# Performance work log

Measured on AMD Instinct MI355X. Metric: run time of the kernel, lower is better.

Reference implementation:

```python
import jax, jax.numpy as jnp
import numpy as np

TOP_K = 2
SCALING = 16.0 / 8.0  # alpha / rank


def setup_inputs() -> dict:
    key = jax.random.key(0)
    ks = jax.random.split(key, 9)
    B, V, D, P = 32, 21, 512, 64
    IN, OUT, E, R, H = D * P, 96, 8, 8, 256
    return {
        "x": jax.random.normal(ks[0], (B, V, D, P), jnp.float32),
        "W_base": jax.random.normal(ks[1], (OUT, IN), jnp.float32) * (IN ** -0.5),
        "b_base": jax.random.normal(ks[2], (OUT,), jnp.float32) * 0.01,
        "W1": jax.random.normal(ks[3], (H, D), jnp.float32) * (D ** -0.5),
        "b1": jax.random.normal(ks[4], (H,), jnp.float32) * 0.01,
        "W2": jax.random.normal(ks[5], (E, H), jnp.float32) * (H ** -0.5),
        "b2": jax.random.normal(ks[6], (E,), jnp.float32) * 0.01,
        "lora_A": jax.random.normal(ks[7], (E, R, IN), jnp.float32) * (IN ** -0.5),
        "lora_B": jax.random.normal(ks[8], (E, OUT, R), jnp.float32) * (R ** -0.5),
    }


def reference(x, W_base, b_base, W1, b1, W2, b2, lora_A, lora_B):
    B, V, D, P = x.shape
    E = lora_A.shape[0]
    # FlattenHead: flatten last two dims, then linear (dropout is identity in eval)
    flat = x.reshape(B, V, D * P)                      # [B, V, IN]
    base_out = flat @ W_base.T + b_base                # [B, V, OUT]
    # Router: pool over n_vars then patch dim -> [B, D]
    pooled = x.mean(axis=1).mean(axis=-1)
    h = jax.nn.relu(pooled @ W1.T + b1)
    logits = h @ W2.T + b2                             # [B, E]
    probs = jax.nn.softmax(logits, axis=-1)
    topw, topi = jax.lax.top_k(probs, TOP_K)           # [B, K]
    topw = topw / jnp.clip(topw.sum(-1, keepdims=True), 1e-6)
    # All LoRA experts (matches original dense compute), then weighted combine
    temp = jnp.einsum("bvi,eri->ebvr", flat, lora_A)   # [E, B, V, R]
    delta = jnp.einsum("ebvr,eor->ebvo", temp, lora_B) * SCALING  # [E, B, V, OUT]
    # Scatter top-k weights into dense [B, E] then combine (top-k sparse combine)
    w_full = jnp.zeros((B, E), x.dtype).at[jnp.arange(B)[:, None], topi].add(topw)
    moe_delta = jnp.einsum("be,ebvo->bvo", w_full, delta)
    return base_out + moe_delta, probs
```

## Files before the change

### kernel.cpp

```cpp
#include <hip/hip_runtime.h>

#define B_DIM 32
#define V_DIM 21
#define D_DIM 512
#define P_DIM 64
#define M_TOTAL 672
#define K_TOTAL 32768
#define OUT_DIM 96
#define E_DIM 8
#define R_DIM 8
#define H_DIM 256
#define N_TOTAL 160
#define SCALING 2.0f
#define POOL_SCALE (1.0f / (V_DIM * (float)P_DIM))

#define BM 64
#define BK 64
#define KSPLIT 64
#define K_PER_SPLIT (K_TOTAL / KSPLIT)
#define CHUNKS (K_PER_SPLIT / BK)
#define LDS_K (BK + 8)
#define SMN (M_TOTAL * N_TOTAL)
#define RC_ROWS 2

typedef __attribute__((ext_vector_type(4))) float floatx4;
typedef __attribute__((ext_vector_type(8))) short short8;
typedef __attribute__((ext_vector_type(4))) short shortx4;

__device__ __forceinline__ unsigned short f2bf(float f) {
  union { float f; unsigned int u; } v; v.f = f;
  unsigned int u = v.u + (0x7FFFu + ((v.u >> 16) & 1u));
  return (unsigned short)(u >> 16);
}

__global__ __launch_bounds__(256)
void convW_kernel(const float* __restrict__ W_base, const float* __restrict__ lora_A,
                  short* __restrict__ Wb, float* __restrict__ pooled) {
  int gid = blockIdx.x * 256 + threadIdx.x;
  if (blockIdx.x < 64) pooled[gid] = 0.0f;
  size_t base = (size_t)gid * 8;
  int row = (int)(base >> 15);
  int k = (int)(base & 32767);
  const float* src = (row < OUT_DIM) ? (W_base + ((size_t)row << 15) + k)
                                     : (lora_A + ((size_t)(row - OUT_DIM) << 15) + k);
  floatx4 v0 = ((const floatx4*)src)[0];
  floatx4 v1 = ((const floatx4*)src)[1];
  short8 sv;
  sv[0] = (short)f2bf(v0[0]); sv[1] = (short)f2bf(v0[1]);
  sv[2] = (short)f2bf(v0[2]); sv[3] = (short)f2bf(v0[3]);
  sv[4] = (short)f2bf(v1[0]); sv[5] = (short)f2bf(v1[1]);
  sv[6] = (short)f2bf(v1[2]); sv[7] = (short)f2bf(v1[3]);
  *(short8*)(Wb + base) = sv;
}

__global__ __launch_bounds__(256, 4)
void gemm_kernel(const float* __restrict__ x, const short* __restrict__ Wb,
                 float* __restrict__ P, float* __restrict__ pooled) {
  __shared__ short ldsA[BM * LDS_K];
  __shared__ short ldsB[N_TOTAL * LDS_K];
  __shared__ float lds_pool[5 * 8];
  const int tid = threadIdx.x;
  const int m0 = blockIdx.x * BM;
  const int ky = blockIdx.y;
  const int kbase = ky * K_PER_SPLIT;
  const int lane = tid & 63;
  const int wave = tid >> 6;
  const int quad = lane >> 4;
  const int l16 = lane & 15;
  const int b_first = m0 / V_DIM;
  const int d_first = kbase >> 6;

  if (tid < 40) lds_pool[tid] = 0.0f;

  floatx4 acc[10];
  #pragma unroll
  for (int nt = 0; nt < 10; ++nt) acc[nt] = (floatx4)(0.0f);

  floatx4 pa[4];
  short8 pb[5];

#define ISSUE(c)                                                                \
  {                                                                             \
    const int kc = kbase + (c) * BK;                                            \
    _Pragma("unroll")                                                           \
    for (int it = 0; it < 4; ++it) {                                            \
      int idx = it * 256 + tid;                                                 \
      int arow = idx >> 4;                                                      \
      int u = idx & 15;                                                         \
      int m = m0 + arow;                                                        \
      pa[it] = (m < M_TOTAL)                                                    \
          ? *(const floatx4*)(x + (size_t)m * K_TOTAL + kc + u * 4)             \
          : (floatx4)(0.0f);                                                    \
    }                                                                           \
    _Pragma("unroll")                                                           \
    for (int it = 0; it < 5; ++it) {                                            \
      int idx = it * 256 + tid;                                                 \
      int brow = idx >> 3;                                                      \
      int g = idx & 7;                                                          \
      pb[it] = *(const short8*)(Wb + (size_t)brow * K_TOTAL + kc + g * 8);      \
    }                                                                           \
  }

#define CONVERT_WRITE(c)                                                        \
  {                                                                             \
    _Pragma("unroll")                                                           \
    for (int it = 0; it < 4; ++it) {                                            \
      int idx = it * 256 + tid;                                                 \
      int arow = idx >> 4;                                                      \
      int u = idx & 15;                                                         \
      int m = m0 + arow;                                                        \
      floatx4 v = pa[it];                                                       \
         \
      float s = (v[0] + v[1]) + (v[2] + v[3]);                                  \
      s += __shfl_down(s, 8, 16);                                               \
      s += __shfl_down(s, 4, 16);                                               \
      s += __shfl_down(s, 2, 16);                                               \
      s += __shfl_down(s, 1, 16);                                               \
      if ((tid & 15) == 0 && m < M_TOTAL) {                                     \
        int b_local = (m / V_DIM) - b_first;                                    \
        atomicAdd(&lds_pool[b_local * 8 + (c)], s);                             \
      }                                                                         \
      shortx4 sv;                                                               \
      sv[0] = (short)f2bf(v[0]); sv[1] = (short)f2bf(v[1]);                     \
      sv[2] = (short)f2bf(v[2]); sv[3] = (short)f2bf(v[3]);                     \
      *(shortx4*)&ldsA[arow * LDS_K + u * 4] = sv;                              \
    }                                                                           \
    _Pragma("unroll")                                                           \
    for (int it = 0; it < 5; ++it) {                                            \
      int idx = it * 256 + tid;                                                 \
      int brow = idx >> 3;                                                      \
      int g = idx & 7;                                                          \
      *(short8*)&ldsB[brow * LDS_K + g * 8] = pb[it];                           \
    }                                                                           \
  }

  ISSUE(0);
  __syncthreads();
  CONVERT_WRITE(0);

  for (int c = 0; c < CHUNKS; ++c) {
    __syncthreads();
    if (c + 1 < CHUNKS) ISSUE(c + 1);
    #pragma unroll
    for (int ks = 0; ks < 2; ++ks) {
      const int ko = ks * 32 + quad * 8;
      short8 a = *(const short8*)&ldsA[(wave * 16 + l16) * LDS_K + ko];
      #pragma unroll
      for (int nt = 0; nt < 10; ++nt) {
        short8 b = *(const short8*)&ldsB[(nt * 16 + l16) * LDS_K + ko];
        acc[nt] = __builtin_amdgcn_mfma_f32_16x16x32_bf16(a, b, acc[nt], 0, 0, 0);
      }
    }
    __syncthreads();
    if (c + 1 < CHUNKS) CONVERT_WRITE(c + 1);
  }

  {
    const int mrow = m0 + wave * 16 + quad * 4;
    float* Pp = P + (size_t)ky * SMN + (size_t)mrow * N_TOTAL + l16;
    #pragma unroll
    for (int r = 0; r < 4; ++r)
      if (mrow + r < M_TOTAL)
        #pragma unroll
        for (int nt = 0; nt < 10; ++nt)
          Pp[(size_t)r * N_TOTAL + nt * 16] = acc[nt][r];
  }

  if (tid < 40) {
    int b = b_first + (tid >> 3);
    int d = d_first + (tid & 7);
    if (b < B_DIM)
      atomicAdd(&pooled[b * D_DIM + d], lds_pool[tid] * POOL_SCALE);
  }
}

__global__ __launch_bounds__(256)
void router_kernel(const float* __restrict__ pooled, const float* __restrict__ W1,
                   const float* __restrict__ b1, const float* __restrict__ W2,
                   const float* __restrict__ b2, float* __restrict__ wfull,
                   float* __restrict__ probs_out) {
  __shared__ float sp[D_DIM];
  __shared__ float sh[H_DIM];
  __shared__ float slog[E_DIM];
  const int b = blockIdx.x;
  const int t = threadIdx.x;
  sp[t] = pooled[b * D_DIM + t];
  sp[t + 256] = pooled[b * D_DIM + t + 256];
  __syncthreads();
  float acc = b1[t];
  const float* w1r = W1 + (size_t)t * D_DIM;
  for (int d = 0; d < D_DIM; ++d) acc += sp[d] * w1r[d];
  sh[t] = fmaxf(acc, 0.0f);
  __syncthreads();
  if (t < E_DIM) {
    float a = b2[t];
    const float* w2r = W2 + t * H_DIM;
    for (int j = 0; j < H_DIM; ++j) a += sh[j] * w2r[j];
    slog[t] = a;
  }
  __syncthreads();
  if (t == 0) {
    float p[E_DIM];
    float mx = slog[0];
    for (int e = 1; e < E_DIM; ++e) mx = fmaxf(mx, slog[e]);
    float se = 0.0f;
    for (int e = 0; e < E_DIM; ++e) { p[e] = __expf(slog[e] - mx); se += p[e]; }
    float inv = 1.0f / se;
    for (int e = 0; e < E_DIM; ++e) { p[e] *= inv; probs_out[b * E_DIM + e] = p[e]; }
    int i0 = 0;
    for (int e = 1; e < E_DIM; ++e) if (p[e] > p[i0]) i0 = e;
    int i1 = (i0 == 0) ? 1 : 0;
    for (int e = 0; e < E_DIM; ++e) if (e != i0 && p[e] > p[i1]) i1 = e;
    float s2 = p[i0] + p[i1];
    float invs = 1.0f / fmaxf(s2, 1e-6f);
    for (int e = 0; e < E_DIM; ++e) {
      float w = 0.0f;
      if (e == i0) w += p[i0] * invs;
      if (e == i1) w += p[i1] * invs;
      wfull[b * E_DIM + e] = w;
    }
  }
}

__global__ __launch_bounds__(256)
void reduce_combine_kernel(const float* __restrict__ P, const float* __restrict__ b_base,
                           const float* __restrict__ lora_B, const float* __restrict__ wfull,
                           float* __restrict__ out) {
  __shared__ float sS[RC_ROWS * N_TOTAL];
  const int t = threadIdx.x;
  const size_t base = (size_t)blockIdx.x * (RC_ROWS * N_TOTAL);
  for (int s = t; s < RC_ROWS * N_TOTAL; s += 256) {
    const float* Pp = P + base + s;
    float a = 0.0f;
    #pragma unroll 8
    for (int k = 0; k < KSPLIT; ++k) a += Pp[(size_t)k * SMN];
    sS[s] = a;
  }
  __syncthreads();
  if (t < RC_ROWS * OUT_DIM) {
    int mr = t / OUT_DIM;
    int o = t - mr * OUT_DIM;
    int mm = blockIdx.x * RC_ROWS + mr;
    int b = mm / V_DIM;
    const float* srow = sS + mr * N_TOTAL;
    float res = srow[o] + b_base[o];
    float moe = 0.0f;
    #pragma unroll
    for (int e = 0; e < E_DIM; ++e) {
      float we = wfull[b * E_DIM + e];
      if (we != 0.0f) {
        const float* lb = lora_B + ((size_t)e * OUT_DIM + o) * R_DIM;
        float dd = 0.0f;
        #pragma unroll
        for (int r = 0; r < R_DIM; ++r) dd += srow[OUT_DIM + e * R_DIM + r] * lb[r];
        moe += we * dd;
      }
    }
    out[(size_t)mm * OUT_DIM + o] = res + SCALING * moe;
  }
}

extern "C" void kernel_launch(void* const* d_in, const int* in_sizes, int n_in,
                              void* d_out, int out_size, void* d_ws, size_t ws_size,
                              hipStream_t stream) {
  const float* x      = (const float*)d_in[0];
  const float* W_base = (const float*)d_in[1];
  const float* b_base = (const float*)d_in[2];
  const float* W1     = (const float*)d_in[3];
  const float* b1     = (const float*)d_in[4];
  const float* W2     = (const float*)d_in[5];
  const float* b2     = (const float*)d_in[6];
  const float* lora_A = (const float*)d_in[7];
  const float* lora_B = (const float*)d_in[8];
  float* out = (float*)d_out;

  float* ws     = (float*)d_ws;
  float* pooled = ws;
  float* wfull  = ws + 16384;
  short* Wb     = (short*)(wfull + 256);
  float* P      = (float*)(Wb + (size_t)N_TOTAL * K_TOTAL);

  convW_kernel<<<(N_TOTAL * K_TOTAL / 8 + 255) / 256, 256, 0, stream>>>(
      W_base, lora_A, Wb, pooled);
  gemm_kernel<<<dim3(11, KSPLIT), 256, 0, stream>>>(x, Wb, P, pooled);
  router_kernel<<<B_DIM, 256, 0, stream>>>(pooled, W1, b1, W2, b2, wfull,
                                           out + (size_t)M_TOTAL * OUT_DIM);
  reduce_combine_kernel<<<M_TOTAL / RC_ROWS, 256, 0, stream>>>(
      P, b_base, lora_B, wfull, out);
}
```

Before: 206.8 us.

## Stream GEMM tiles directly to LDS with async loads and double buffering

Replaces the register-staged global loads and LDS writes with global_load_lds direct-to-LDS copies into double-buffered, XOR-swizzled LDS tiles. The A tile stays fp32 in LDS and is converted to bf16 with packed cvt instructions right before the MFMAs. The pooling reduction now reads from LDS instead of registers. BK shrinks to 32, so there are twice as many iterations and barriers. The aim is to cut VGPR pressure and overlap memory with compute, at the cost of more LDS traffic for the fp32 A tile and more synchronisation.

```diff
diff --git a/kernel.cpp b/kernel.cpp
--- a/kernel.cpp
+++ b/kernel.cpp
@@ -15,22 +15,32 @@
 #define POOL_SCALE (1.0f / (V_DIM * (float)P_DIM))
 
 #define BM 64
-#define BK 64
+#define BK 32
 #define KSPLIT 64
 #define K_PER_SPLIT (K_TOTAL / KSPLIT)
 #define CHUNKS (K_PER_SPLIT / BK)
-#define LDS_K (BK + 8)
 #define SMN (M_TOTAL * N_TOTAL)
 #define RC_ROWS 2
 
 typedef __attribute__((ext_vector_type(4))) float floatx4;
 typedef __attribute__((ext_vector_type(8))) short short8;
-typedef __attribute__((ext_vector_type(4))) short shortx4;
 
 __device__ __forceinline__ unsigned short f2bf(float f) {
   union { float f; unsigned int u; } v; v.f = f;
   unsigned int u = v.u + (0x7FFFu + ((v.u >> 16) & 1u));
   return (unsigned short)(u >> 16);
+}
+
+__device__ __forceinline__ unsigned int cvt_pk_bf16(float lo, float hi) {
+  unsigned int r;
+  asm("v_cvt_pk_bf16_f32 %0, %1, %2" : "=v"(r) : "v"(lo), "v"(hi));
+  return r;
+}
+
+__device__ __forceinline__ void gl_lds16(const void* g, void* l) {
+  __builtin_amdgcn_global_load_lds(
+      (const __attribute__((address_space(1))) void*)g,
+      (__attribute__((address_space(3))) void*)l, 16, 0, 0);
 }
 
 __global__ __launch_bounds__(256)
@@ -56,9 +66,10 @@
 __global__ __launch_bounds__(256, 4)
 void gemm_kernel(const float* __restrict__ x, const short* __restrict__ Wb,
                  float* __restrict__ P, float* __restrict__ pooled) {
-  __shared__ short ldsA[BM * LDS_K];
-  __shared__ short ldsB[N_TOTAL * LDS_K];
+  __shared__ __attribute__((aligned(16))) float ldsA[2][BM * BK];
+  __shared__ __attribute__((aligned(16))) short ldsB[2][N_TOTAL * BK];
   __shared__ float lds_pool[5 * 8];
+
   const int tid = threadIdx.x;
   const int m0 = blockIdx.x * BM;
   const int ky = blockIdx.y;
@@ -72,87 +83,91 @@
 
   if (tid < 40) lds_pool[tid] = 0.0f;
 
+  const float* srcA[2];
+  int dstA[2];
+  #pragma unroll
+  for (int it = 0; it < 2; ++it) {
+    int idx = it * 256 + tid;
+    int row = idx >> 3, j = idx & 7;
+    int m = m0 + row; if (m > M_TOTAL - 1) m = M_TOTAL - 1;
+    srcA[it] = x + (size_t)m * K_TOTAL + kbase + ((j ^ (row & 7)) << 2);
+    dstA[it] = (it * 256 + (tid & 192)) << 2;
+  }
+  const short* srcB[3];
+  int dstB[3];
+  #pragma unroll
+  for (int it = 0; it < 3; ++it) {
+    int idx = it * 256 + tid;
+    if (idx < 640) {
+      int pair = idx >> 3, s8 = idx & 7;
+      int c8 = s8 ^ (pair & 7);
+      int row = pair * 2 + (c8 >> 2), j = c8 & 3;
+      srcB[it] = Wb + (size_t)row * K_TOTAL + kbase + (j << 3);
+      dstB[it] = (it * 256 + (tid & 192)) << 3;
+    } else {
+      srcB[it] = Wb; dstB[it] = 0;
+    }
+  }
+
+  const int prow = tid >> 2;
+  const int part = tid & 3;
+  const int ps1 = (prow + part) & 7;
+  const int ps2 = (ps1 + 4) & 7;
+  const int pm = m0 + prow;
+  const int pool_base = (pm < M_TOTAL) ? ((pm / V_DIM) - b_first) * 8 : -1;
+
+#define ISSUE(c, bb)                                                          \
+  {                                                                           \
+    _Pragma("unroll")                                                         \
+    for (int it = 0; it < 2; ++it)                                            \
+      gl_lds16(srcA[it] + (c) * BK, &ldsA[bb][dstA[it]]);                     \
+    _Pragma("unroll")                                                         \
+    for (int it = 0; it < 2; ++it)                                            \
+      gl_lds16(srcB[it] + (c) * BK, &ldsB[bb][dstB[it]]);                     \
+    if (tid < 128) gl_lds16(srcB[2] + (c) * BK, &ldsB[bb][dstB[2]]);          \
+  }
+
   floatx4 acc[10];
   #pragma unroll
   for (int nt = 0; nt < 10; ++nt) acc[nt] = (floatx4)(0.0f);
 
-  floatx4 pa[4];
-  short8 pb[5];
-
-#define ISSUE(c)                                                                \
-  {                                                                             \
-    const int kc = kbase + (c) * BK;                                            \
-    _Pragma("unroll")                                                           \
-    for (int it = 0; it < 4; ++it) {                                            \
-      int idx = it * 256 + tid;                                                 \
-      int arow = idx >> 4;                                                      \
-      int u = idx & 15;                                                         \
-      int m = m0 + arow;                                                        \
-      pa[it] = (m < M_TOTAL)                                                    \
-          ? *(const floatx4*)(x + (size_t)m * K_TOTAL + kc + u * 4)             \
-          : (floatx4)(0.0f);                                                    \
-    }                                                                           \
-    _Pragma("unroll")                                                           \
-    for (int it = 0; it < 5; ++it) {                                            \
-      int idx = it * 256 + tid;                                                 \
-      int brow = idx >> 3;                                                      \
-      int g = idx & 7;                                                          \
-      pb[it] = *(const short8*)(Wb + (size_t)brow * K_TOTAL + kc + g * 8);      \
-    }                                                                           \
-  }
-
-#define CONVERT_WRITE(c)                                                        \
-  {                                                                             \
-    _Pragma("unroll")                                                           \
-    for (int it = 0; it < 4; ++it) {                                            \
-      int idx = it * 256 + tid;                                                 \
-      int arow = idx >> 4;                                                      \
-      int u = idx & 15;                                                         \
-      int m = m0 + arow;                                                        \
-      floatx4 v = pa[it];                                                       \
-         \
-      float s = (v[0] + v[1]) + (v[2] + v[3]);                                  \
-      s += __shfl_down(s, 8, 16);                                               \
-      s += __shfl_down(s, 4, 16);                                               \
-      s += __shfl_down(s, 2, 16);                                               \
-      s += __shfl_down(s, 1, 16);                                               \
-      if ((tid & 15) == 0 && m < M_TOTAL) {                                     \
-        int b_local = (m / V_DIM) - b_first;                                    \
-        atomicAdd(&lds_pool[b_local * 8 + (c)], s);                             \
-      }                                                                         \
-      shortx4 sv;                                                               \
-      sv[0] = (short)f2bf(v[0]); sv[1] = (short)f2bf(v[1]);                     \
-      sv[2] = (short)f2bf(v[2]); sv[3] = (short)f2bf(v[3]);                     \
-      *(shortx4*)&ldsA[arow * LDS_K + u * 4] = sv;                              \
-    }                                                                           \
-    _Pragma("unroll")                                                           \
-    for (int it = 0; it < 5; ++it) {                                            \
-      int idx = it * 256 + tid;                                                 \
-      int brow = idx >> 3;                                                      \
-      int g = idx & 7;                                                          \
-      *(short8*)&ldsB[brow * LDS_K + g * 8] = pb[it];                           \
-    }                                                                           \
-  }
-
-  ISSUE(0);
-  __syncthreads();
-  CONVERT_WRITE(0);
-
+  ISSUE(0, 0);
+  __syncthreads();
+
+  #pragma unroll
   for (int c = 0; c < CHUNKS; ++c) {
-    __syncthreads();
-    if (c + 1 < CHUNKS) ISSUE(c + 1);
-    #pragma unroll
-    for (int ks = 0; ks < 2; ++ks) {
-      const int ko = ks * 32 + quad * 8;
-      short8 a = *(const short8*)&ldsA[(wave * 16 + l16) * LDS_K + ko];
+    const int buf = c & 1;
+    if (c + 1 < CHUNKS) ISSUE(c + 1, buf ^ 1);
+    {
+      const floatx4* aT = (const floatx4*)ldsA[buf];
+      floatx4 u = aT[prow * 8 + ps1];
+      floatx4 w = aT[prow * 8 + ps2];
+      float s = ((u[0] + u[1]) + (u[2] + u[3])) + ((w[0] + w[1]) + (w[2] + w[3]));
+      s += __shfl_down(s, 2, 4);
+      s += __shfl_down(s, 1, 4);
+      if (part == 0 && pool_base >= 0)
+        atomicAdd(&lds_pool[pool_base + (c >> 1)], s);
+    }
+    {
+      const floatx4* aT = (const floatx4*)ldsA[buf];
+      const int r = wave * 16 + l16;
+      floatx4 f0 = aT[r * 8 + ((2 * quad) ^ (r & 7))];
+      floatx4 f1 = aT[r * 8 + ((2 * quad + 1) ^ (r & 7))];
+      union { short8 s; unsigned int u[4]; } av;
+      av.u[0] = cvt_pk_bf16(f0[0], f0[1]);
+      av.u[1] = cvt_pk_bf16(f0[2], f0[3]);
+      av.u[2] = cvt_pk_bf16(f1[0], f1[1]);
+      av.u[3] = cvt_pk_bf16(f1[2], f1[3]);
+      const short8* bT = (const short8*)ldsB[buf];
       #pragma unroll
       for (int nt = 0; nt < 10; ++nt) {
-        short8 b = *(const short8*)&ldsB[(nt * 16 + l16) * LDS_K + ko];
-        acc[nt] = __builtin_amdgcn_mfma_f32_16x16x32_bf16(a, b, acc[nt], 0, 0, 0);
+        int r2 = nt * 16 + l16;
+        int pr = r2 >> 1;
+        short8 b = bT[pr * 8 + ((((r2 & 1) << 2) | quad) ^ (pr & 7))];
+        acc[nt] = __builtin_amdgcn_mfma_f32_16x16x32_bf16(av.s, b, acc[nt], 0, 0, 0);
       }
     }
     __syncthreads();
-    if (c + 1 < CHUNKS) CONVERT_WRITE(c + 1);
   }
 
   {
```

Result: no change. 206.1 us (-0.4%).
